# Performance work log

Hardware: AMD Instinct MI355X
Metric: run time of the kernel (lower is better)

Reference implementation:

```python
import jax, jax.numpy as jnp
import numpy as np

B, S, H = 1, 2048, 2048
E, I = 16, 1408
I_SHARED = 5632
TOP_K = 2


def setup_inputs() -> dict:
    key = jax.random.key(0)
    ks = jax.random.split(key, 8)
    scale = 0.02
    return {
        "hidden_states": jax.random.normal(ks[0], (B, S, H), dtype=jnp.float32),
        "router_w": jax.random.normal(ks[1], (H, E), dtype=jnp.float32) * scale,
        "expert_gate_up_w": jax.random.normal(ks[2], (E, H, 2 * I), dtype=jnp.float32) * scale,
        "expert_out_w": jax.random.normal(ks[3], (E, I, H), dtype=jnp.float32) * scale,
        "shared_ffw_gate_w": jax.random.normal(ks[4], (H, I_SHARED), dtype=jnp.float32) * scale,
        "shared_ffw_inter_w": jax.random.normal(ks[5], (H, I_SHARED), dtype=jnp.float32) * scale,
        "shared_ffw_out_w": jax.random.normal(ks[6], (I_SHARED, H), dtype=jnp.float32) * scale,
        "shared_gate_w": jax.random.normal(ks[7], (H, 1), dtype=jnp.float32) * scale,
        "top_k": TOP_K,
    }


def reference(hidden_states, router_w, expert_gate_up_w, expert_out_w,
              shared_ffw_gate_w, shared_ffw_inter_w, shared_ffw_out_w,
              shared_gate_w, top_k):
    b, s, h = hidden_states.shape
    e = router_w.shape[-1]
    x = hidden_states.reshape(-1, h)  # [T, H]

    # --- Router: softmax over experts, top-k, renormalize (norm_top_k_prob=True) ---
    router_logits = x @ router_w                        # [T, E]
    router_probs = jax.nn.softmax(router_logits, -1)
    top_p, top_i = jax.lax.top_k(router_probs, top_k)   # [T, K]
    top_p = top_p / jnp.sum(top_p, axis=-1, keepdims=True)
    # dense routing matrix [E, T] (matches one_hot-sum-transpose in source)
    one_hot = jax.nn.one_hot(top_i, e, dtype=top_p.dtype)  # [T, K, E]
    routing_full = jnp.sum(one_hot * top_p[..., None], axis=1).T  # [E, T]

    # --- Dense per-expert SwiGLU over ALL tokens (as in QwenMoeExperts) ---
    gate_up = jnp.einsum('th,ehm->etm', x, expert_gate_up_w)  # [E, T, 2I]
    gate, up = jnp.split(gate_up, 2, axis=-1)
    hidden = up * jax.nn.silu(gate)                           # [E, T, I]
    expert_out = jnp.einsum('eti,eih->eth', hidden, expert_out_w)  # [E, T, H]
    expert_contribution = jnp.einsum('eth,et->th', expert_out, routing_full)

    # --- Shared expert (SwiGLU MLP) with sigmoid gate ---
    sgate = jax.nn.silu(x @ shared_ffw_gate_w)
    sinter = x @ shared_ffw_inter_w
    shared_out = (sinter * sgate) @ shared_ffw_out_w          # [T, H]
    shared_out = shared_out * jax.nn.sigmoid(x @ shared_gate_w)

    out = (expert_contribution + shared_out).reshape(b, s, h)
    return out, router_logits
```

## Files before the change

### kernel.cpp

```cpp
#include <hip/hip_runtime.h>
#include <math.h>

typedef __attribute__((ext_vector_type(4))) float f32x4;
typedef __attribute__((ext_vector_type(2))) unsigned int u32x2;
typedef __attribute__((ext_vector_type(4))) unsigned int u32x4;
typedef __attribute__((ext_vector_type(8))) unsigned short u16x8;
typedef __attribute__((ext_vector_type(8))) __bf16 bf16x8;
typedef unsigned short ushort_t;

#define H_DIM 2048
#define T_TOK 2048
#define NEXP 16
#define I_DIM 1408
#define I2_DIM 2816
#define IS_DIM 5632
#define MAXROWS 6144

static __device__ __forceinline__ unsigned short f2bf(float f){
  union { float f; unsigned u; } v; v.f = f;
  unsigned r = v.u + 0x7FFFu + ((v.u >> 16) & 1u);
  return (unsigned short)(r >> 16);
}
static __device__ __forceinline__ float bf2f(unsigned short h){
  union { unsigned u; float f; } v; v.u = ((unsigned)h) << 16;
  return v.f;
}
static __device__ __forceinline__ float silu_f(float x){ return x / (1.f + __expf(-x)); }

static __device__ __forceinline__ void gld16(const ushort_t* g, ushort_t* l){
  __builtin_amdgcn_global_load_lds(
      (const __attribute__((address_space(1))) unsigned int*)g,
      (__attribute__((address_space(3))) unsigned int*)l, 16, 0, 0);
}

__global__ void cast_bf16_k(const float* __restrict__ in, ushort_t* __restrict__ out){
  long i = ((long)blockIdx.x * 256 + threadIdx.x) * 8;
  f32x4 a = *(const f32x4*)&in[i];
  f32x4 b = *(const f32x4*)&in[i + 4];
  union { ushort_t s[8]; u32x4 v; } pk;
  #pragma unroll
  for (int j = 0; j < 4; j++){ pk.s[j] = f2bf(a[j]); pk.s[j+4] = f2bf(b[j]); }
  *(u32x4*)&out[i] = pk.v;
}

__global__ void transpose_cast_k(const float* __restrict__ in, ushort_t* __restrict__ out,
                                 int K, int N){
  long zo = (long)blockIdx.z * K * N;
  in += zo; out += zo;
  __shared__ float tl[32][33];
  int n0 = blockIdx.x * 32, k0 = blockIdx.y * 32;
  int tid = threadIdx.x;
  int tx = tid & 31, ty = tid >> 5;
  #pragma unroll
  for (int j = 0; j < 4; j++)
    tl[ty + j*8][tx] = in[(long)(k0 + ty + j*8) * N + n0 + tx];
  __syncthreads();
  int nl = tid >> 3, kc = (tid & 7) * 4;
  unsigned w0 = (unsigned)f2bf(tl[kc+0][nl]) | ((unsigned)f2bf(tl[kc+1][nl]) << 16);
  unsigned w1 = (unsigned)f2bf(tl[kc+2][nl]) | ((unsigned)f2bf(tl[kc+3][nl]) << 16);
  u32x2 o; o[0] = w0; o[1] = w1;
  *(u32x2*)&out[(long)(n0 + nl) * K + k0 + kc] = o;
}

__global__ void router_k(const float* __restrict__ x, const float* __restrict__ rw,
                         const float* __restrict__ sgw, float* __restrict__ logits,
                         int* __restrict__ counts, int* __restrict__ lists,
                         float* __restrict__ probs, float* __restrict__ sgmul){
  int wid = threadIdx.x >> 6, lane = threadIdx.x & 63;
  int t = blockIdx.x * 4 + wid;
  const float* xr = x + (long)t * H_DIM;
  float acc[17];
  #pragma unroll
  for (int e = 0; e < 17; e++) acc[e] = 0.f;
  for (int h0 = lane * 4; h0 < H_DIM; h0 += 256){
    f32x4 xv = *(const f32x4*)&xr[h0];
    #pragma unroll
    for (int i = 0; i < 4; i++){
      float xs = xv[i];
      const float* wrow = rw + (long)(h0 + i) * NEXP;
      #pragma unroll
      for (int e = 0; e < 16; e++) acc[e] += xs * wrow[e];
      acc[16] += xs * sgw[h0 + i];
    }
  }
  #pragma unroll
  for (int e = 0; e < 17; e++)
    for (int off = 32; off >= 1; off >>= 1)
      acc[e] += __shfl_xor(acc[e], off);
  if (lane == 0){
    float* lo = logits + (long)t * NEXP;
    #pragma unroll
    for (int e = 0; e < 16; e++) lo[e] = acc[e];
    int e0 = 0;
    #pragma unroll
    for (int e = 1; e < 16; e++) if (acc[e] > acc[e0]) e0 = e;
    int e1 = (e0 == 0) ? 1 : 0;
    #pragma unroll
    for (int e = 0; e < 16; e++) if (e != e0 && acc[e] > acc[e1]) e1 = e;
    float d = acc[e1] - acc[e0];
    float ed = __expf(d);
    float p0 = 1.f / (1.f + ed);
    float p1 = ed / (1.f + ed);
    int pos0 = atomicAdd(&counts[e0], 1);
    lists[e0 * T_TOK + pos0] = t; probs[e0 * T_TOK + pos0] = p0;
    int pos1 = atomicAdd(&counts[e1], 1);
    lists[e1 * T_TOK + pos1] = t; probs[e1 * T_TOK + pos1] = p1;
    sgmul[t] = 1.f / (1.f + __expf(-acc[16]));
  }
}

__global__ void bases_k(const int* __restrict__ counts, int* __restrict__ bases){
  if (threadIdx.x == 0){
    int r = 0;
    for (int e = 0; e < NEXP; e++){ bases[e] = r; r += (counts[e] + 127) & ~127; }
  }
}

__global__ void swiglu_expert_k(const ushort_t* __restrict__ gu, ushort_t* __restrict__ hid){
  long qd = (long)blockIdx.x * 256 + threadIdx.x;
  long r = qd / (I_DIM / 8); int ic = (int)(qd % (I_DIM / 8)) * 8;
  const ushort_t* g = gu + r * I2_DIM + ic;
  u16x8 gv = *(const u16x8*)g;
  u16x8 uv = *(const u16x8*)(g + I_DIM);
  u16x8 ov;
  #pragma unroll
  for (int i = 0; i < 8; i++)
    ov[i] = f2bf(bf2f(uv[i]) * silu_f(bf2f(gv[i])));
  *(u16x8*)&hid[r * I_DIM + ic] = ov;
}

__global__ void swiglu_flat_k(ushort_t* __restrict__ sg, const ushort_t* __restrict__ si){
  long i = ((long)blockIdx.x * 256 + threadIdx.x) * 8;
  u16x8 g = *(const u16x8*)&sg[i];
  u16x8 s = *(const u16x8*)&si[i];
  u16x8 o;
  #pragma unroll
  for (int j = 0; j < 8; j++)
    o[j] = f2bf(bf2f(s[j]) * silu_f(bf2f(g[j])));
  *(u16x8*)&sg[i] = o;
}

template<int MODE>
__global__ __launch_bounds__(256)
void gemm_k(const ushort_t* __restrict__ A, const ushort_t* __restrict__ Bt,
            const ushort_t* __restrict__ Bt2, ushort_t* __restrict__ Cb,
            int K, int lda, int ldbt, int ldc, int mb,
            const int* __restrict__ counts, const int* __restrict__ bases,
            const int* __restrict__ lists, const float* __restrict__ probs,
            const float* __restrict__ svec, float* __restrict__ outp,
            long bstride){
  int z = blockIdx.z;
  int cnt = T_TOK;
  const ushort_t* Ab = A;
  const ushort_t* Bb = Bt;
  long rbase = 0;
  if constexpr (MODE == 0){ if (z){ Bb = Bt2; Cb += (long)T_TOK * ldc; } }
  if constexpr (MODE == 1){ cnt = counts[z]; rbase = bases[z]; Bb += (long)z * bstride; }
  if constexpr (MODE == 2){ cnt = counts[z]; Ab += (long)bases[z] * lda; Bb += (long)z * bstride; }

  int kb = K / gridDim.y;
  int kbase = blockIdx.y * kb;
  Ab += kbase;
  Bb += kbase;

  int nwg = gridDim.x;
  int wgo = blockIdx.x;
  int q = nwg >> 3, r = nwg & 7;
  int xcd = wgo & 7, idx = wgo >> 3;
  int wg = (xcd < r ? xcd * (q + 1) : r * (q + 1) + (xcd - r) * q) + idx;
  int mblk = wg % mb, nblk = wg / mb;
  int m0 = mblk * 128;
  if (m0 >= cnt) return;
  int n0 = nblk * 128;

  __shared__ ushort_t As[128 * 32];
  __shared__ ushort_t Bs[128 * 32];

  int tid = threadIdx.x;
  int lane = tid & 63;
  int wv = tid >> 6;
  int wr = wv >> 1, wc = wv & 1;

  int crow = lane >> 2;
  int kcol = (lane & 3) * 8;
  long aoff[2], boff[2];
  ushort_t* lA[2]; ushort_t* lB[2];
  #pragma unroll
  for (int c = 0; c < 2; c++){
    int mr = wv * 32 + c * 16 + crow;
    int grow;
    if constexpr (MODE == 1){
      int j = m0 + mr; if (j >= cnt) j = cnt - 1;
      grow = lists[z * T_TOK + j];
    } else {
      grow = m0 + mr;
    }
    aoff[c] = (long)grow * lda + kcol;
    boff[c] = (long)(n0 + mr) * ldbt + kcol;
    lA[c] = As + (wv * 32 + c * 16) * 32;
    lB[c] = Bs + (wv * 32 + c * 16) * 32;
  }

  f32x4 zero = {0.f, 0.f, 0.f, 0.f};
  f32x4 acc[4][4];
  #pragma unroll
  for (int i = 0; i < 4; i++)
    #pragma unroll
    for (int j = 0; j < 4; j++) acc[i][j] = zero;

  int nsteps = kb >> 5;
  for (int s = 0; s < nsteps; s++){
    __syncthreads();
    int kof = s * 32;
    gld16(Ab + aoff[0] + kof, lA[0]);
    gld16(Ab + aoff[1] + kof, lA[1]);
    gld16(Bb + boff[0] + kof, lB[0]);
    gld16(Bb + boff[1] + kof, lB[1]);
    __syncthreads();
    bf16x8 af[4], bg[4];
    #pragma unroll
    for (int f = 0; f < 4; f++){
      af[f] = *(const bf16x8*)&As[(wr*64 + f*16 + (lane & 15)) * 32 + (lane >> 4) * 8];
      bg[f] = *(const bf16x8*)&Bs[(wc*64 + f*16 + (lane & 15)) * 32 + (lane >> 4) * 8];
    }
    #pragma unroll
    for (int fm = 0; fm < 4; fm++)
      #pragma unroll
      for (int fn = 0; fn < 4; fn++)
        acc[fm][fn] = __builtin_amdgcn_mfma_f32_16x16x32_bf16(af[fm], bg[fn], acc[fm][fn], 0, 0, 0);
  }

  int colb = n0 + wc * 64 + (lane & 15);
  int rowb = m0 + wr * 64 + (lane >> 4) * 4;
  #pragma unroll
  for (int fm = 0; fm < 4; fm++){
    #pragma unroll
    for (int fn = 0; fn < 4; fn++){
      f32x4 v = acc[fm][fn];
      int col = colb + fn * 16;
      #pragma unroll
      for (int rr = 0; rr < 4; rr++){
        int m = rowb + fm * 16 + rr;
        if constexpr (MODE == 0){
          Cb[(long)m * ldc + col] = f2bf(v[rr]);
        } else if constexpr (MODE == 1){
          if (m < cnt) Cb[(rbase + m) * (long)ldc + col] = f2bf(v[rr]);
        } else if constexpr (MODE == 2){
          if (m < cnt){
            int tok = lists[z * T_TOK + m];
            float pp = probs[z * T_TOK + m];
            atomicAdd(outp + (long)tok * ldc + col, pp * v[rr]);
          }
        } else {
          atomicAdd(outp + (long)m * ldc + col, svec[m] * v[rr]);
        }
      }
    }
  }
}

extern "C" void kernel_launch(void* const* d_in, const int* in_sizes, int n_in,
                              void* d_out, int out_size, void* d_ws, size_t ws_size,
                              hipStream_t stream){
  const float* x    = (const float*)d_in[0];
  const float* rw   = (const float*)d_in[1];
  const float* wgu  = (const float*)d_in[2];
  const float* wout = (const float*)d_in[3];
  const float* wsg  = (const float*)d_in[4];
  const float* wsi  = (const float*)d_in[5];
  const float* wso  = (const float*)d_in[6];
  const float* sgw  = (const float*)d_in[7];

  float* out = (float*)d_out;
  float* logits = out + (size_t)T_TOK * H_DIM;

  char* w = (char*)d_ws;
  auto alloc = [&](size_t b){ char* p = w; w += (b + 255) & ~(size_t)255; return p; };
  ushort_t* xb     = (ushort_t*)alloc((size_t)T_TOK * H_DIM * 2);
  ushort_t* wgu_t  = (ushort_t*)alloc((size_t)NEXP * I2_DIM * H_DIM * 2);
  ushort_t* wout_t = (ushort_t*)alloc((size_t)NEXP * H_DIM * I_DIM * 2);
  ushort_t* wsg_t  = (ushort_t*)alloc((size_t)IS_DIM * H_DIM * 2);
  ushort_t* wsi_t  = (ushort_t*)alloc((size_t)IS_DIM * H_DIM * 2);
  ushort_t* wso_t  = (ushort_t*)alloc((size_t)H_DIM * IS_DIM * 2);
  ushort_t* sgr    = (ushort_t*)alloc((size_t)2 * T_TOK * IS_DIM * 2);
  ushort_t* sir    = sgr + (size_t)T_TOK * IS_DIM;
  ushort_t* gu     = (ushort_t*)alloc((size_t)MAXROWS * I2_DIM * 2);
  ushort_t* hid    = (ushort_t*)alloc((size_t)MAXROWS * I_DIM * 2);
  int*   counts = (int*)alloc(64);
  int*   bases  = (int*)alloc(64);
  int*   lists  = (int*)alloc((size_t)NEXP * T_TOK * 4);
  float* probs  = (float*)alloc((size_t)NEXP * T_TOK * 4);
  float* sgmul  = (float*)alloc((size_t)T_TOK * 4);

  hipMemsetAsync(counts, 0, 64, stream);
  hipMemsetAsync(out, 0, (size_t)T_TOK * H_DIM * sizeof(float), stream);

  cast_bf16_k<<<2048, 256, 0, stream>>>(x, xb);
  transpose_cast_k<<<dim3(I2_DIM/32, H_DIM/32, NEXP), 256, 0, stream>>>(wgu, wgu_t, H_DIM, I2_DIM);
  transpose_cast_k<<<dim3(H_DIM/32, I_DIM/32, NEXP), 256, 0, stream>>>(wout, wout_t, I_DIM, H_DIM);
  transpose_cast_k<<<dim3(IS_DIM/32, H_DIM/32, 1), 256, 0, stream>>>(wsg, wsg_t, H_DIM, IS_DIM);
  transpose_cast_k<<<dim3(IS_DIM/32, H_DIM/32, 1), 256, 0, stream>>>(wsi, wsi_t, H_DIM, IS_DIM);
  transpose_cast_k<<<dim3(H_DIM/32, IS_DIM/32, 1), 256, 0, stream>>>(wso, wso_t, IS_DIM, H_DIM);

  router_k<<<512, 256, 0, stream>>>(x, rw, sgw, logits, counts, lists, probs, sgmul);
  bases_k<<<1, 64, 0, stream>>>(counts, bases);

  gemm_k<0><<<dim3((IS_DIM/128) * (T_TOK/128), 1, 2), 256, 0, stream>>>(
      xb, wsg_t, wsi_t, sgr, H_DIM, H_DIM, H_DIM, IS_DIM, T_TOK/128,
      nullptr, nullptr, nullptr, nullptr, nullptr, nullptr, 0);
  swiglu_flat_k<<<(T_TOK * (IS_DIM/8)) / 256, 256, 0, stream>>>(sgr, sir);
  gemm_k<3><<<dim3((H_DIM/128) * (T_TOK/128), 2, 1), 256, 0, stream>>>(
      sgr, wso_t, nullptr, nullptr, IS_DIM, IS_DIM, IS_DIM, H_DIM, T_TOK/128,
      nullptr, nullptr, nullptr, nullptr, sgmul, out, 0);

  gemm_k<1><<<dim3((I2_DIM/128) * (T_TOK/128), 1, NEXP), 256, 0, stream>>>(
      xb, wgu_t, nullptr, gu, H_DIM, H_DIM, H_DIM, I2_DIM, T_TOK/128,
      counts, bases, lists, probs, nullptr, nullptr, (long)I2_DIM * H_DIM);
  swiglu_expert_k<<<(MAXROWS * (I_DIM/8)) / 256, 256, 0, stream>>>(gu, hid);
  gemm_k<2><<<dim3((H_DIM/128) * (T_TOK/128), 1, NEXP), 256, 0, stream>>>(
      hid, wout_t, nullptr, nullptr, I_DIM, I_DIM, I_DIM, H_DIM, T_TOK/128,
      counts, bases, lists, probs, nullptr, out, (long)H_DIM * I_DIM);

  (void)in_sizes; (void)n_in; (void)out_size; (void)ws_size;
}
```

Baseline: 861.6 us.

## Rewrite GEMM with 256x256 tiles, double-buffered swizzled LDS and 512 threads

Replaces the 128x128 single-buffered GEMM with a 256x256-tile kernel using 8 waves and K-steps of 64. It double-buffers the LDS loads so the next tile is fetched while the current one is computed, and applies an XOR swizzle to avoid LDS bank conflicts. The aim is more data reuse per byte loaded and fewer barriers per unit of work. The expert row padding and MAXROWS grow to fit the larger M tile. In exchange it uses 128KB of dynamic LDS, so only one block fits per CU, and it adds more padded work for experts with few tokens.

```diff
diff --git a/kernel.cpp b/kernel.cpp
--- a/kernel.cpp
+++ b/kernel.cpp
@@ -14,7 +14,7 @@
 #define I_DIM 1408
 #define I2_DIM 2816
 #define IS_DIM 5632
-#define MAXROWS 6144
+#define MAXROWS 8192
 
 static __device__ __forceinline__ unsigned short f2bf(float f){
   union { float f; unsigned u; } v; v.f = f;
@@ -112,7 +112,7 @@
 __global__ void bases_k(const int* __restrict__ counts, int* __restrict__ bases){
   if (threadIdx.x == 0){
     int r = 0;
-    for (int e = 0; e < NEXP; e++){ bases[e] = r; r += (counts[e] + 127) & ~127; }
+    for (int e = 0; e < NEXP; e++){ bases[e] = r; r += (counts[e] + 255) & ~255; }
   }
 }
 
@@ -141,14 +141,14 @@
 }
 
 template<int MODE>
-__global__ __launch_bounds__(256)
-void gemm_k(const ushort_t* __restrict__ A, const ushort_t* __restrict__ Bt,
-            const ushort_t* __restrict__ Bt2, ushort_t* __restrict__ Cb,
-            int K, int lda, int ldbt, int ldc, int mb,
-            const int* __restrict__ counts, const int* __restrict__ bases,
-            const int* __restrict__ lists, const float* __restrict__ probs,
-            const float* __restrict__ svec, float* __restrict__ outp,
-            long bstride){
+__global__ __launch_bounds__(512, 2)
+void gemm2_k(const ushort_t* __restrict__ A, const ushort_t* __restrict__ Bt,
+             const ushort_t* __restrict__ Bt2, ushort_t* __restrict__ Cb,
+             int K, int lda, int ldbt, int ldc, int mb,
+             const int* __restrict__ counts, const int* __restrict__ bases,
+             const int* __restrict__ lists, const float* __restrict__ probs,
+             const float* __restrict__ svec, float* __restrict__ outp,
+             long bstride){
   int z = blockIdx.z;
   int cnt = T_TOK;
   const ushort_t* Ab = A;
@@ -168,26 +168,23 @@
   int q = nwg >> 3, r = nwg & 7;
   int xcd = wgo & 7, idx = wgo >> 3;
   int wg = (xcd < r ? xcd * (q + 1) : r * (q + 1) + (xcd - r) * q) + idx;
-  int mblk = wg % mb, nblk = wg / mb;
-  int m0 = mblk * 128;
+  int m0 = (wg % mb) * 256;
   if (m0 >= cnt) return;
-  int n0 = nblk * 128;
-
-  __shared__ ushort_t As[128 * 32];
-  __shared__ ushort_t Bs[128 * 32];
+  int n0 = (wg / mb) * 256;
+
+  extern __shared__ ushort_t lds[];
 
   int tid = threadIdx.x;
   int lane = tid & 63;
   int wv = tid >> 6;
-  int wr = wv >> 1, wc = wv & 1;
-
-  int crow = lane >> 2;
-  int kcol = (lane & 3) * 8;
-  long aoff[2], boff[2];
-  ushort_t* lA[2]; ushort_t* lB[2];
-  #pragma unroll
-  for (int c = 0; c < 2; c++){
-    int mr = wv * 32 + c * 16 + crow;
+  int wm = wv >> 2;
+  int wn = wv & 3;
+
+  int sg = ((lane & 7) ^ (lane >> 3)) * 8;
+  long aoff[4], boff[4];
+  #pragma unroll
+  for (int i = 0; i < 4; i++){
+    int mr = wv * 32 + i * 8 + (lane >> 3);
     int grow;
     if constexpr (MODE == 1){
       int j = m0 + mr; if (j >= cnt) j = cnt - 1;
@@ -195,45 +192,64 @@
     } else {
       grow = m0 + mr;
     }
-    aoff[c] = (long)grow * lda + kcol;
-    boff[c] = (long)(n0 + mr) * ldbt + kcol;
-    lA[c] = As + (wv * 32 + c * 16) * 32;
-    lB[c] = Bs + (wv * 32 + c * 16) * 32;
-  }
+    aoff[i] = (long)grow * lda + sg;
+    boff[i] = (long)(n0 + mr) * ldbt + sg;
+  }
+  ushort_t* stA = lds + (size_t)(wv * 32) * 64;
+  ushort_t* stB = lds + 16384 + (size_t)(wv * 32) * 64;
 
   f32x4 zero = {0.f, 0.f, 0.f, 0.f};
-  f32x4 acc[4][4];
-  #pragma unroll
-  for (int i = 0; i < 4; i++)
+  f32x4 acc[8][4];
+  #pragma unroll
+  for (int i = 0; i < 8; i++)
     #pragma unroll
     for (int j = 0; j < 4; j++) acc[i][j] = zero;
 
-  int nsteps = kb >> 5;
-  for (int s = 0; s < nsteps; s++){
-    __syncthreads();
-    int kof = s * 32;
-    gld16(Ab + aoff[0] + kof, lA[0]);
-    gld16(Ab + aoff[1] + kof, lA[1]);
-    gld16(Bb + boff[0] + kof, lB[0]);
-    gld16(Bb + boff[1] + kof, lB[1]);
-    __syncthreads();
-    bf16x8 af[4], bg[4];
-    #pragma unroll
-    for (int f = 0; f < 4; f++){
-      af[f] = *(const bf16x8*)&As[(wr*64 + f*16 + (lane & 15)) * 32 + (lane >> 4) * 8];
-      bg[f] = *(const bf16x8*)&Bs[(wc*64 + f*16 + (lane & 15)) * 32 + (lane >> 4) * 8];
-    }
-    #pragma unroll
-    for (int fm = 0; fm < 4; fm++)
+  int nt = kb >> 6;
+  #pragma unroll
+  for (int i = 0; i < 4; i++){
+    gld16(Ab + aoff[i], stA + i * 512);
+    gld16(Bb + boff[i], stB + i * 512);
+  }
+  __syncthreads();
+
+  int c = 0;
+  for (int t = 0; t < nt; t++){
+    if (t + 1 < nt){
+      long ko = (long)(t + 1) * 64;
+      int nb = (c ^ 1) * 32768;
+      #pragma unroll
+      for (int i = 0; i < 4; i++){
+        gld16(Ab + aoff[i] + ko, stA + nb + i * 512);
+        gld16(Bb + boff[i] + ko, stB + nb + i * 512);
+      }
+    }
+    const ushort_t* tA = lds + c * 32768;
+    const ushort_t* tB = tA + 16384;
+    #pragma unroll
+    for (int kk = 0; kk < 2; kk++){
+      int cs = ((kk * 4 + (lane >> 4)) ^ (lane & 7)) * 8;
+      bf16x8 af[8], bf[4];
+      #pragma unroll
+      for (int fm = 0; fm < 8; fm++)
+        af[fm] = *(const bf16x8*)&tA[(wm*128 + fm*16 + (lane & 15)) * 64 + cs];
       #pragma unroll
       for (int fn = 0; fn < 4; fn++)
-        acc[fm][fn] = __builtin_amdgcn_mfma_f32_16x16x32_bf16(af[fm], bg[fn], acc[fm][fn], 0, 0, 0);
-  }
-
-  int colb = n0 + wc * 64 + (lane & 15);
-  int rowb = m0 + wr * 64 + (lane >> 4) * 4;
-  #pragma unroll
-  for (int fm = 0; fm < 4; fm++){
+        bf[fn] = *(const bf16x8*)&tB[(wn*64 + fn*16 + (lane & 15)) * 64 + cs];
+      #pragma unroll
+      for (int fm = 0; fm < 8; fm++)
+        #pragma unroll
+        for (int fn = 0; fn < 4; fn++)
+          acc[fm][fn] = __builtin_amdgcn_mfma_f32_16x16x32_bf16(af[fm], bf[fn], acc[fm][fn], 0, 0, 0);
+    }
+    if (t + 1 < nt) __syncthreads();
+    c ^= 1;
+  }
+
+  int colb = n0 + wn * 64 + (lane & 15);
+  int rowb = m0 + wm * 128 + (lane >> 4) * 4;
+  #pragma unroll
+  for (int fm = 0; fm < 8; fm++){
     #pragma unroll
     for (int fn = 0; fn < 4; fn++){
       f32x4 v = acc[fm][fn];
@@ -305,21 +321,23 @@
   router_k<<<512, 256, 0, stream>>>(x, rw, sgw, logits, counts, lists, probs, sgmul);
   bases_k<<<1, 64, 0, stream>>>(counts, bases);
 
-  gemm_k<0><<<dim3((IS_DIM/128) * (T_TOK/128), 1, 2), 256, 0, stream>>>(
-      xb, wsg_t, wsi_t, sgr, H_DIM, H_DIM, H_DIM, IS_DIM, T_TOK/128,
+  const size_t LDSB = 2 * 2 * 256 * 64 * sizeof(ushort_t);
+
+  gemm2_k<0><<<dim3((T_TOK/256) * (IS_DIM/256), 1, 2), 512, LDSB, stream>>>(
+      xb, wsg_t, wsi_t, sgr, H_DIM, H_DIM, H_DIM, IS_DIM, T_TOK/256,
       nullptr, nullptr, nullptr, nullptr, nullptr, nullptr, 0);
   swiglu_flat_k<<<(T_TOK * (IS_DIM/8)) / 256, 256, 0, stream>>>(sgr, sir);
-  gemm_k<3><<<dim3((H_DIM/128) * (T_TOK/128), 2, 1), 256, 0, stream>>>(
-      sgr, wso_t, nullptr, nullptr, IS_DIM, IS_DIM, IS_DIM, H_DIM, T_TOK/128,
+  gemm2_k<3><<<dim3((T_TOK/256) * (H_DIM/256), 4, 1), 512, LDSB, stream>>>(
+      sgr, wso_t, nullptr, nullptr, IS_DIM, IS_DIM, IS_DIM, H_DIM, T_TOK/256,
       nullptr, nullptr, nullptr, nullptr, sgmul, out, 0);
 
-  gemm_k<1><<<dim3((I2_DIM/128) * (T_TOK/128), 1, NEXP), 256, 0, stream>>>(
-      xb, wgu_t, nullptr, gu, H_DIM, H_DIM, H_DIM, I2_DIM, T_TOK/128,
+  gemm2_k<1><<<dim3((T_TOK/256) * (I2_DIM/256), 1, NEXP), 512, LDSB, stream>>>(
+      xb, wgu_t, nullptr, gu, H_DIM, H_DIM, H_DIM, I2_DIM, T_TOK/256,
       counts, bases, lists, probs, nullptr, nullptr, (long)I2_DIM * H_DIM);
-  swiglu_expert_k<<<(MAXROWS * (I_DIM/8)) / 256, 256, 0, stream>>>(gu, hid);
-  gemm_k<2><<<dim3((H_DIM/128) * (T_TOK/128), 1, NEXP), 256, 0, stream>>>(
-      hid, wout_t, nullptr, nullptr, I_DIM, I_DIM, I_DIM, H_DIM, T_TOK/128,
-      counts, bases, lists, probs, nullptr, out, (long)H_DIM * I_DIM);
+  swiglu_expert_k<<<((long)MAXROWS * (I_DIM/8)) / 256, 256, 0, stream>>>(gu, hid);
+  gemm2_k<2><<<dim3((T_TOK/256) * (H_DIM/256), 1, NEXP), 512, LDSB, stream>>>(
+      hid, wout_t, nullptr, nullptr, I_DIM, I_DIM, I_DIM, H_DIM, T_TOK/256,
+      counts, bases, lists, probs, nullptr, out, (long)I_DIM * H_DIM);
 
   (void)in_sizes; (void)n_in; (void)out_size; (void)ws_size;
 }
```

Result: no change. 878.1 us (+1.9%).
